# Performance work log

Hardware: AMD Instinct MI355X
Metric: run time of the kernel (lower is better)

The kernel has to match this reference:

```python
import jax, jax.numpy as jnp
import numpy as np

D_MODEL = 768
N_HEADS = 12
D_HEAD = D_MODEL // N_HEADS


def setup_inputs() -> dict:
    key = jax.random.key(0)
    k1, k2, k3 = jax.random.split(key, 3)
    B, N = 32, 1024
    x = jax.random.normal(k1, (B, N, D_MODEL), dtype=jnp.float32)
    w_qkv = jax.random.normal(k2, (D_MODEL, 3 * D_MODEL), dtype=jnp.float32) * (D_MODEL ** -0.5)
    b_qkv = jnp.zeros((3 * D_MODEL,), dtype=jnp.float32)
    w_proj = jax.random.normal(k3, (D_MODEL, D_MODEL), dtype=jnp.float32) * (D_MODEL ** -0.5)
    b_proj = jnp.zeros((D_MODEL,), dtype=jnp.float32)
    return {"x": x, "w_qkv": w_qkv, "b_qkv": b_qkv, "w_proj": w_proj, "b_proj": b_proj}


def reference(x, w_qkv, b_qkv, w_proj, b_proj):
    B, N, C = x.shape
    H, Dh = N_HEADS, D_HEAD
    # qkv projection: (B,N,3C) -> (3,B,H,N,Dh)
    qkv = (x @ w_qkv + b_qkv).reshape(B, N, 3, H, Dh).transpose(2, 0, 3, 1, 4)
    q, k, v = qkv[0], qkv[1], qkv[2]
    scale = Dh ** -0.5
    attn = jnp.einsum('bhnd,bhmd->bhnm', q, k) * scale  # (B,H,N,N)
    attn = jax.nn.softmax(attn, axis=-1)
    out = jnp.einsum('bhnm,bhmd->bhnd', attn, v)  # (B,H,N,Dh)
    out = out.transpose(0, 2, 1, 3).reshape(B, N, C)
    return out @ w_proj + b_proj
```

## Files before the change

kernel.cpp:

```cpp
#include <hip/hip_runtime.h>
#include <hip/hip_bf16.h>
#include <math.h>

#define BQ   32
#define SEQ  1024
#define DM   768
#define NH   12
#define DH   64
#define CQKV 2304
#define MROWS (BQ * SEQ)
#define NT   12

#define QSCALE 0.1803368801f

typedef __attribute__((ext_vector_type(8))) short  short8;
typedef __attribute__((ext_vector_type(4))) short  short4v;
typedef __attribute__((ext_vector_type(4))) float  floatx4;

using bf16 = __hip_bfloat16;

#define G2L(g, l) __builtin_amdgcn_global_load_lds(                              \
        (const __attribute__((address_space(1))) void*)(g),                      \
        (__attribute__((address_space(3))) void*)(l), 16, 0, 0)

#define WAVE_SYNC() __builtin_amdgcn_wave_barrier()
#define MFMA16(a, b, c) __builtin_amdgcn_mfma_f32_16x16x32_bf16((a), (b), (c), 0, 0, 0)

__global__ void cast_f32_bf16(const float* __restrict__ in, bf16* __restrict__ out,
                              int n4)
{
    int idx = blockIdx.x * blockDim.x + threadIdx.x;
    if (idx < n4) {
        float4 v = ((const float4*)in)[idx];
        bf16 o[4] = { __float2bfloat16(v.x), __float2bfloat16(v.y),
                      __float2bfloat16(v.z), __float2bfloat16(v.w) };
        ((ushort4*)out)[idx] = *(const ushort4*)o;
    }
}

__global__ void transpose_cast(const float* __restrict__ in, bf16* __restrict__ out,
                               int R, int C)
{
    int idx = blockIdx.x * blockDim.x + threadIdx.x;
    if (idx < R * C) {
        int r = idx / C, c = idx % C;
        out[(size_t)c * R + r] = __float2bfloat16(in[idx]);
    }
}

__device__ __forceinline__ void mainloop256(
    const bf16* __restrict__ X, const bf16* __restrict__ WT,
    int m0, int n0, int w, int lane, int lr, int lq,
    bf16 (*Asm)[256][64], bf16 (*Bsm)[128][64], floatx4 acc[4][4])
{
    const int wm = (w >> 1) * 64, wn = (w & 1) * 64;
    const int sr = lane >> 3;
    const int ss = ((lane & 7) ^ sr) * 8;
    const bf16* gA = X  + (size_t)(m0 + w * 8 + sr) * DM + ss;
    const bf16* gB = WT + (size_t)(n0 + w * 8 + sr) * DM + ss;

    auto stage = [&](int T) {
        const int bI = T % 3;
        #pragma unroll
        for (int r = 0; r < 4; ++r)
            G2L(gA + (size_t)(r * 64) * DM + T * 64, &Asm[bI][r * 64 + w * 8][0]);
        #pragma unroll
        for (int r = 0; r < 2; ++r)
            G2L(gB + (size_t)(r * 64) * DM + T * 64, &Bsm[bI][r * 64 + w * 8][0]);
    };

    stage(0); stage(1);

    #pragma unroll
    for (int T = 0; T < NT; ++T) {
        if (T + 2 < NT) stage(T + 2);
        if      (T < NT - 2)  asm volatile("s_waitcnt vmcnt(12)" ::: "memory");
        else if (T == NT - 2) asm volatile("s_waitcnt vmcnt(6)"  ::: "memory");
        else                  asm volatile("s_waitcnt vmcnt(0)"  ::: "memory");
        __builtin_amdgcn_s_barrier();
        asm volatile("" ::: "memory");

        const int bI = T % 3;
        short8 af[4][2], bfr[4][2];
        #pragma unroll
        for (int m = 0; m < 4; ++m)
            #pragma unroll
            for (int ks = 0; ks < 2; ++ks)
                af[m][ks] = *(const short8*)(
                    &Asm[bI][wm + m * 16 + lr][((ks * 4 + lq) ^ (lr & 7)) * 8]);
        #pragma unroll
        for (int n = 0; n < 4; ++n)
            #pragma unroll
            for (int ks = 0; ks < 2; ++ks)
                bfr[n][ks] = *(const short8*)(
                    &Bsm[bI][wn + n * 16 + lr][((ks * 4 + lq) ^ (lr & 7)) * 8]);

        __builtin_amdgcn_s_setprio(1);
        #pragma unroll
        for (int ks = 0; ks < 2; ++ks)
            #pragma unroll
            for (int m = 0; m < 4; ++m)
                #pragma unroll
                for (int n = 0; n < 4; ++n)
                    acc[m][n] = MFMA16(af[m][ks], bfr[n][ks], acc[m][n]);
        __builtin_amdgcn_s_setprio(0);

        asm volatile("" ::: "memory");
        __builtin_amdgcn_s_barrier();
        asm volatile("" ::: "memory");
    }
}

__global__ __launch_bounds__(512, 2) void gemm_qkv(
    const bf16* __restrict__ X, const bf16* __restrict__ WT,
    const float* __restrict__ bias,
    bf16* __restrict__ Qo, bf16* __restrict__ Ko, bf16* __restrict__ Vt)
{
    extern __shared__ __align__(16) char smem[];
    auto Asm = (bf16(*)[256][64])smem;
    auto Bsm = (bf16(*)[128][64])(smem + 3 * 256 * 64 * 2);
    auto Es  = (bf16(*)[32][72])smem;

    const int t = threadIdx.x, w = t >> 6, lane = t & 63;
    const int lr = lane & 15, lq = lane >> 4;
    const int id = blockIdx.x;
    const int xcd = id & 7, o = id >> 3;
    const int m0 = (xcd * 16 + o / 18) * 256;
    const int n0 = (o % 18) * 128;

    floatx4 acc[4][4] = {};
    mainloop256(X, WT, m0, n0, w, lane, lr, lq, Asm, Bsm, acc);

    const int wm = (w >> 1) * 64, wn = (w & 1) * 64;
    const int cb = n0 + wn;
    const int which = cb / DM;
    const int hb    = (cb % DM) / DH;
    const int nbw   = m0 + wm;
    const int bb    = nbw >> 10, nloc = nbw & (SEQ - 1);
    const size_t head = (size_t)bb * NH + hb;
    const float qmul = (which == 0) ? QSCALE : 1.0f;

    if (which != 2) {
        bf16* Out = (which ? Ko : Qo) + (head * SEQ + nloc) * DH;
        #pragma unroll
        for (int c2 = 0; c2 < 2; ++c2) {
            #pragma unroll
            for (int ah = 0; ah < 2; ++ah) {
                const int at = c2 * 2 + ah;
                #pragma unroll
                for (int bt = 0; bt < 4; ++bt) {
                    const float bv = bias[cb + bt * 16 + lr];
                    #pragma unroll
                    for (int rr = 0; rr < 4; ++rr)
                        Es[w][ah * 16 + lq * 4 + rr][bt * 16 + lr] =
                            __float2bfloat16((acc[at][bt][rr] + bv) * qmul);
                }
            }
            WAVE_SYNC();
            #pragma unroll
            for (int i = 0; i < 4; ++i) {
                const int r = i * 8 + (lane >> 3), s = lane & 7;
                short8 vv = *(const short8*)(&Es[w][r][s * 8]);
                *(short8*)(Out + (size_t)(c2 * 32 + r) * DH + s * 8) = vv;
            }
            WAVE_SYNC();
        }
    } else {
        bf16* Out = Vt + head * DH * SEQ + nloc;
        #pragma unroll
        for (int c2 = 0; c2 < 2; ++c2) {
            #pragma unroll
            for (int bh = 0; bh < 2; ++bh) {
                const int bt = c2 * 2 + bh;
                const float bv = bias[cb + bt * 16 + lr];
                #pragma unroll
                for (int at = 0; at < 4; ++at)
                    #pragma unroll
                    for (int rr = 0; rr < 4; ++rr)
                        Es[w][bh * 16 + lr][at * 16 + lq * 4 + rr] =
                            __float2bfloat16(acc[at][bt][rr] + bv);
            }
            WAVE_SYNC();
            #pragma unroll
            for (int i = 0; i < 4; ++i) {
                const int r = i * 8 + (lane >> 3), s = lane & 7;
                short8 vv = *(const short8*)(&Es[w][r][s * 8]);
                *(short8*)(Out + (size_t)(c2 * 32 + r) * SEQ + s * 8) = vv;
            }
            WAVE_SYNC();
        }
    }
}

__global__ __launch_bounds__(512, 2) void gemm_proj(
    const bf16* __restrict__ A, const bf16* __restrict__ WT,
    const float* __restrict__ bias, float* __restrict__ out)
{
    extern __shared__ __align__(16) char smem[];
    auto Asm = (bf16(*)[256][64])smem;
    auto Bsm = (bf16(*)[128][64])(smem + 3 * 256 * 64 * 2);

    const int t = threadIdx.x, w = t >> 6, lane = t & 63;
    const int lr = lane & 15, lq = lane >> 4;
    const int id = blockIdx.x;
    const int xcd = id & 7, o = id >> 3;
    const int m0 = (xcd * 16 + o / 6) * 256;
    const int n0 = (o % 6) * 128;

    floatx4 acc[4][4] = {};
    mainloop256(A, WT, m0, n0, w, lane, lr, lq, Asm, Bsm, acc);

    const int wm = (w >> 1) * 64, wn = (w & 1) * 64;
    #pragma unroll
    for (int bt = 0; bt < 4; ++bt) {
        const float bv = bias[n0 + wn + bt * 16 + lr];
        #pragma unroll
        for (int at = 0; at < 4; ++at) {
            const int rg = m0 + wm + at * 16 + lq * 4;
            #pragma unroll
            for (int rr = 0; rr < 4; ++rr)
                out[(size_t)(rg + rr) * DM + n0 + wn + bt * 16 + lr] =
                    acc[at][bt][rr] + bv;
        }
    }
}

__global__ __launch_bounds__(256) void flash_attn(
    const bf16* __restrict__ Q, const bf16* __restrict__ K,
    const bf16* __restrict__ Vt, bf16* __restrict__ O)
{
    __shared__ __align__(16) bf16 Ks[2][2][64][32];
    __shared__ __align__(16) bf16 Vs[2][2][64][32];
    __shared__ __align__(16) bf16 Plds[4][32][72];
    const int w = threadIdx.x >> 6, lane = threadIdx.x & 63;
    const int lr = lane & 15, lq = lane >> 4;

    const int fid = blockIdx.x;
    const int g   = (fid & 7) + ((fid >> 6) << 3);
    const int x   = (fid >> 3) & 7;
    const int h   = g % NH, b = g / NH;
    const int qb  = x * 128 + w * 32;

    const bf16* Qh = Q  + (size_t)(b * NH + h) * SEQ * DH;
    const bf16* Kh = K  + (size_t)(b * NH + h) * SEQ * DH;
    const bf16* Vh = Vt + (size_t)(b * NH + h) * DH * SEQ;

    short8 bq[2][2];
    #pragma unroll
    for (int qs = 0; qs < 2; ++qs) {
        bq[qs][0] = *(const short8*)(Qh + (size_t)(qb + qs * 16 + lr) * DH + lq * 8);
        bq[qs][1] = *(const short8*)(Qh + (size_t)(qb + qs * 16 + lr) * DH + 32 + lq * 8);
    }

    floatx4 acc[2][4] = {};
    floatx4 lsum[2] = {};

    const int srow = lane >> 2;
    const int ssw  = ((lane & 3) ^ ((lane >> 3) & 3)) * 8;
    const int rsw  = (lr >> 1) & 3;

    const bf16* gsrc[4];
    bf16*       ldst[4];
    #pragma unroll
    for (int i = 0; i < 4; ++i) {
        const int idx = w * 4 + i;
        if (idx < 8) {
            const int hh = idx >> 2, gg = idx & 3;
            gsrc[i] = Kh + (size_t)(gg * 16 + srow) * DH + hh * 32 + ssw;
            ldst[i] = &Ks[0][hh][gg * 16][0];
        } else {
            const int vv = idx - 8, hh = vv >> 2, gg = vv & 3;
            gsrc[i] = Vh + (size_t)(gg * 16 + srow) * SEQ + hh * 32 + ssw;
            ldst[i] = &Vs[0][hh][gg * 16][0];
        }
    }
    const int gstep = (w < 2) ? 64 * DH : 64;

    auto stage = [&](int bi) {
        #pragma unroll
        for (int i = 0; i < 4; ++i) {
            G2L(gsrc[i], ldst[i] + bi * 4096);
            gsrc[i] += gstep;
        }
    };

    stage(0);
    __syncthreads();

    int cur = 0;
    for (int j0 = 0; j0 < SEQ; j0 += 64) {
        if (j0 + 64 < SEQ) stage(cur ^ 1);

        short8 ak[4][2];
        #pragma unroll
        for (int jt = 0; jt < 4; ++jt) {
            ak[jt][0] = *(const short8*)(&Ks[cur][0][jt * 16 + lr][(lq ^ rsw) * 8]);
            ak[jt][1] = *(const short8*)(&Ks[cur][1][jt * 16 + lr][(lq ^ rsw) * 8]);
        }
        #pragma unroll
        for (int qs = 0; qs < 2; ++qs) {
            #pragma unroll
            for (int jt = 0; jt < 4; ++jt) {
                floatx4 c = {};
                c = MFMA16(ak[jt][0], bq[qs][0], c);
                c = MFMA16(ak[jt][1], bq[qs][1], c);
                bf16 pk[4];
                #pragma unroll
                for (int r = 0; r < 4; ++r) {
                    float p = __builtin_amdgcn_exp2f(c[r]);
                    lsum[qs][r] += p;
                    pk[r] = __float2bfloat16(p);
                }
                *(short4v*)(&Plds[w][qs * 16 + lr][jt * 16 + lq * 4]) =
                    *(const short4v*)pk;
            }
        }
        WAVE_SYNC();

        short8 bv[4][2];
        #pragma unroll
        for (int dt = 0; dt < 4; ++dt) {
            bv[dt][0] = *(const short8*)(&Vs[cur][0][dt * 16 + lr][(lq ^ rsw) * 8]);
            bv[dt][1] = *(const short8*)(&Vs[cur][1][dt * 16 + lr][(lq ^ rsw) * 8]);
        }
        __builtin_amdgcn_s_setprio(1);
        #pragma unroll
        for (int qs = 0; qs < 2; ++qs) {
            short8 ap0 = *(const short8*)(&Plds[w][qs * 16 + lr][lq * 8]);
            short8 ap1 = *(const short8*)(&Plds[w][qs * 16 + lr][32 + lq * 8]);
            #pragma unroll
            for (int dt = 0; dt < 4; ++dt) {
                acc[qs][dt] = MFMA16(ap0, bv[dt][0], acc[qs][dt]);
                acc[qs][dt] = MFMA16(ap1, bv[dt][1], acc[qs][dt]);
            }
        }
        __builtin_amdgcn_s_setprio(0);

        __syncthreads();
        cur ^= 1;
    }

    float li[2];
    #pragma unroll
    for (int qs = 0; qs < 2; ++qs) {
        li[qs] = (lsum[qs][0] + lsum[qs][1]) + (lsum[qs][2] + lsum[qs][3]);
        li[qs] += __shfl_xor(li[qs], 16);
        li[qs] += __shfl_xor(li[qs], 32);
    }
    #pragma unroll
    for (int qs = 0; qs < 2; ++qs) {
        float inv[4];
        #pragma unroll
        for (int r = 0; r < 4; ++r)
            inv[r] = 1.f / __shfl(li[qs], lq * 4 + r);
        #pragma unroll
        for (int dt = 0; dt < 4; ++dt)
            #pragma unroll
            for (int r = 0; r < 4; ++r) {
                const int qi = qb + qs * 16 + lq * 4 + r;
                O[((size_t)b * SEQ + qi) * DM + h * DH + dt * 16 + lr] =
                    __float2bfloat16(acc[qs][dt][r] * inv[r]);
            }
    }
}

extern "C" void kernel_launch(void* const* d_in, const int* in_sizes, int n_in,
                              void* d_out, int out_size, void* d_ws, size_t ws_size,
                              hipStream_t stream)
{
    const float* x      = (const float*)d_in[0];
    const float* w_qkv  = (const float*)d_in[1];
    const float* b_qkv  = (const float*)d_in[2];
    const float* w_proj = (const float*)d_in[3];
    const float* b_proj = (const float*)d_in[4];
    float* out = (float*)d_out;

    bf16* ws = (bf16*)d_ws;
    size_t off = 0;
    bf16* wqkvT  = ws + off; off += (size_t)CQKV * DM;
    bf16* wprojT = ws + off; off += (size_t)DM * DM;
    bf16* Xb  = ws + off; off += (size_t)MROWS * DM;
    bf16* Qb  = ws + off; off += (size_t)BQ * NH * SEQ * DH;
    bf16* Kb  = ws + off; off += (size_t)BQ * NH * SEQ * DH;
    bf16* Vtb = ws + off; off += (size_t)BQ * NH * DH * SEQ;
    bf16* Ob  = ws + off; off += (size_t)MROWS * DM;

    static bool attr_done = false;
    if (!attr_done) {
        (void)hipFuncSetAttribute((const void*)gemm_qkv,
                hipFuncAttributeMaxDynamicSharedMemorySize, 147456);
        (void)hipFuncSetAttribute((const void*)gemm_proj,
                hipFuncAttributeMaxDynamicSharedMemorySize, 147456);
        attr_done = true;
    }

    cast_f32_bf16<<<(MROWS * DM / 4 + 255) / 256, 256, 0, stream>>>(x, Xb, MROWS * DM / 4);
    transpose_cast<<<(DM * CQKV + 255) / 256, 256, 0, stream>>>(w_qkv, wqkvT, DM, CQKV);
    transpose_cast<<<(DM * DM + 255) / 256, 256, 0, stream>>>(w_proj, wprojT, DM, DM);
    gemm_qkv<<<dim3(2304), 512, 147456, stream>>>(Xb, wqkvT, b_qkv, Qb, Kb, Vtb);
    flash_attn<<<dim3(BQ * NH * (SEQ / 128)), 256, 0, stream>>>(Qb, Kb, Vtb, Ob);
    gemm_proj<<<dim3(768), 512, 147456, stream>>>(Ob, wprojT, b_proj, out);
}
```

Measured before the change: 505.6 us.

## Enlarge GEMM tiles to 256x256 with double-buffered LDS staging

Both projection GEMMs move from 256x128 block tiles with triple-buffered LDS to 256x256 tiles with double buffering. Each wave now owns a 128x64 sub-tile with an 8x4 accumulator array, and the QKV and projection epilogues, including the transposed V store, are rewritten for the new mapping. The goal is more MFMA work per loaded byte and fewer blocks. In exchange, prefetch depth drops, register pressure rises, and the projection grid becomes 384 blocks, which may leave a partial-wave tail.

```diff
diff --git a/kernel.cpp b/kernel.cpp
--- a/kernel.cpp
+++ b/kernel.cpp
@@ -51,55 +51,57 @@
 __device__ __forceinline__ void mainloop256(
     const bf16* __restrict__ X, const bf16* __restrict__ WT,
     int m0, int n0, int w, int lane, int lr, int lq,
-    bf16 (*Asm)[256][64], bf16 (*Bsm)[128][64], floatx4 acc[4][4])
-{
-    const int wm = (w >> 1) * 64, wn = (w & 1) * 64;
+    bf16 (*Asm)[256][64], bf16 (*Bsm)[256][64], floatx4 acc[8][4])
+{
+    const int wm = (w >> 2) * 128, wn = (w & 3) * 64;
+    const int lr7 = lr & 7;
     const int sr = lane >> 3;
     const int ss = ((lane & 7) ^ sr) * 8;
     const bf16* gA = X  + (size_t)(m0 + w * 8 + sr) * DM + ss;
     const bf16* gB = WT + (size_t)(n0 + w * 8 + sr) * DM + ss;
 
     auto stage = [&](int T) {
-        const int bI = T % 3;
+        const int bI = T & 1;
         #pragma unroll
         for (int r = 0; r < 4; ++r)
             G2L(gA + (size_t)(r * 64) * DM + T * 64, &Asm[bI][r * 64 + w * 8][0]);
         #pragma unroll
-        for (int r = 0; r < 2; ++r)
+        for (int r = 0; r < 4; ++r)
             G2L(gB + (size_t)(r * 64) * DM + T * 64, &Bsm[bI][r * 64 + w * 8][0]);
     };
 
-    stage(0); stage(1);
+    stage(0);
 
     #pragma unroll
     for (int T = 0; T < NT; ++T) {
-        if (T + 2 < NT) stage(T + 2);
-        if      (T < NT - 2)  asm volatile("s_waitcnt vmcnt(12)" ::: "memory");
-        else if (T == NT - 2) asm volatile("s_waitcnt vmcnt(6)"  ::: "memory");
-        else                  asm volatile("s_waitcnt vmcnt(0)"  ::: "memory");
+        if (T + 1 < NT) {
+            stage(T + 1);
+            asm volatile("s_waitcnt vmcnt(8)" ::: "memory");
+        } else {
+            asm volatile("s_waitcnt vmcnt(0)" ::: "memory");
+        }
         __builtin_amdgcn_s_barrier();
         asm volatile("" ::: "memory");
 
-        const int bI = T % 3;
-        short8 af[4][2], bfr[4][2];
-        #pragma unroll
-        for (int m = 0; m < 4; ++m)
-            #pragma unroll
-            for (int ks = 0; ks < 2; ++ks)
+        const int bI = T & 1;
+        short8 af[8][2], bfr[4][2];
+        #pragma unroll
+        for (int ks = 0; ks < 2; ++ks) {
+            #pragma unroll
+            for (int m = 0; m < 8; ++m)
                 af[m][ks] = *(const short8*)(
-                    &Asm[bI][wm + m * 16 + lr][((ks * 4 + lq) ^ (lr & 7)) * 8]);
-        #pragma unroll
-        for (int n = 0; n < 4; ++n)
-            #pragma unroll
-            for (int ks = 0; ks < 2; ++ks)
+                    &Asm[bI][wm + m * 16 + lr][((ks * 4 + lq) ^ lr7) * 8]);
+            #pragma unroll
+            for (int n = 0; n < 4; ++n)
                 bfr[n][ks] = *(const short8*)(
-                    &Bsm[bI][wn + n * 16 + lr][((ks * 4 + lq) ^ (lr & 7)) * 8]);
+                    &Bsm[bI][wn + n * 16 + lr][((ks * 4 + lq) ^ lr7) * 8]);
+        }
 
         __builtin_amdgcn_s_setprio(1);
         #pragma unroll
         for (int ks = 0; ks < 2; ++ks)
             #pragma unroll
-            for (int m = 0; m < 4; ++m)
+            for (int m = 0; m < 8; ++m)
                 #pragma unroll
                 for (int n = 0; n < 4; ++n)
                     acc[m][n] = MFMA16(af[m][ks], bfr[n][ks], acc[m][n]);
@@ -118,20 +120,20 @@
 {
     extern __shared__ __align__(16) char smem[];
     auto Asm = (bf16(*)[256][64])smem;
-    auto Bsm = (bf16(*)[128][64])(smem + 3 * 256 * 64 * 2);
-    auto Es  = (bf16(*)[32][72])smem;
+    auto Bsm = (bf16(*)[256][64])(smem + 2 * 256 * 64 * 2);
+    auto Es  = (bf16(*)[64][72])smem;
 
     const int t = threadIdx.x, w = t >> 6, lane = t & 63;
     const int lr = lane & 15, lq = lane >> 4;
     const int id = blockIdx.x;
     const int xcd = id & 7, o = id >> 3;
-    const int m0 = (xcd * 16 + o / 18) * 256;
-    const int n0 = (o % 18) * 128;
-
-    floatx4 acc[4][4] = {};
+    const int m0 = (xcd * 16 + o / 9) * 256;
+    const int n0 = (o % 9) * 256;
+
+    floatx4 acc[8][4] = {};
     mainloop256(X, WT, m0, n0, w, lane, lr, lq, Asm, Bsm, acc);
 
-    const int wm = (w >> 1) * 64, wn = (w & 1) * 64;
+    const int wm = (w >> 2) * 128, wn = (w & 3) * 64;
     const int cb = n0 + wn;
     const int which = cb / DM;
     const int hb    = (cb % DM) / DH;
@@ -143,17 +145,17 @@
     if (which != 2) {
         bf16* Out = (which ? Ko : Qo) + (head * SEQ + nloc) * DH;
         #pragma unroll
-        for (int c2 = 0; c2 < 2; ++c2) {
+        for (int c2 = 0; c2 < 4; ++c2) {
             #pragma unroll
             for (int ah = 0; ah < 2; ++ah) {
-                const int at = c2 * 2 + ah;
+                const int m = c2 * 2 + ah;
                 #pragma unroll
-                for (int bt = 0; bt < 4; ++bt) {
-                    const float bv = bias[cb + bt * 16 + lr];
+                for (int n = 0; n < 4; ++n) {
+                    const float bv = bias[cb + n * 16 + lr];
                     #pragma unroll
                     for (int rr = 0; rr < 4; ++rr)
-                        Es[w][ah * 16 + lq * 4 + rr][bt * 16 + lr] =
-                            __float2bfloat16((acc[at][bt][rr] + bv) * qmul);
+                        Es[w][ah * 16 + lq * 4 + rr][n * 16 + lr] =
+                            __float2bfloat16((acc[m][n][rr] + bv) * qmul);
                 }
             }
             WAVE_SYNC();
@@ -166,26 +168,27 @@
             WAVE_SYNC();
         }
     } else {
-        bf16* Out = Vt + head * DH * SEQ + nloc;
-        #pragma unroll
-        for (int c2 = 0; c2 < 2; ++c2) {
-            #pragma unroll
-            for (int bh = 0; bh < 2; ++bh) {
-                const int bt = c2 * 2 + bh;
-                const float bv = bias[cb + bt * 16 + lr];
+        bf16* Out = Vt + head * (size_t)(DH * SEQ) + nloc;
+        #pragma unroll
+        for (int mc = 0; mc < 4; ++mc) {
+            #pragma unroll
+            for (int ah = 0; ah < 2; ++ah) {
+                const int m = mc * 2 + ah;
                 #pragma unroll
-                for (int at = 0; at < 4; ++at)
+                for (int n = 0; n < 4; ++n) {
+                    const float bv = bias[cb + n * 16 + lr];
                     #pragma unroll
                     for (int rr = 0; rr < 4; ++rr)
-                        Es[w][bh * 16 + lr][at * 16 + lq * 4 + rr] =
-                            __float2bfloat16(acc[at][bt][rr] + bv);
+                        Es[w][n * 16 + lr][ah * 16 + lq * 4 + rr] =
+                            __float2bfloat16(acc[m][n][rr] + bv);
+                }
             }
             WAVE_SYNC();
             #pragma unroll
             for (int i = 0; i < 4; ++i) {
-                const int r = i * 8 + (lane >> 3), s = lane & 7;
+                const int r = i * 16 + (lane >> 2), s = lane & 3;
                 short8 vv = *(const short8*)(&Es[w][r][s * 8]);
-                *(short8*)(Out + (size_t)(c2 * 32 + r) * SEQ + s * 8) = vv;
+                *(short8*)(Out + (size_t)r * SEQ + mc * 32 + s * 8) = vv;
             }
             WAVE_SYNC();
         }
@@ -198,29 +201,29 @@
 {
     extern __shared__ __align__(16) char smem[];
     auto Asm = (bf16(*)[256][64])smem;
-    auto Bsm = (bf16(*)[128][64])(smem + 3 * 256 * 64 * 2);
+    auto Bsm = (bf16(*)[256][64])(smem + 2 * 256 * 64 * 2);
 
     const int t = threadIdx.x, w = t >> 6, lane = t & 63;
     const int lr = lane & 15, lq = lane >> 4;
     const int id = blockIdx.x;
     const int xcd = id & 7, o = id >> 3;
-    const int m0 = (xcd * 16 + o / 6) * 256;
-    const int n0 = (o % 6) * 128;
-
-    floatx4 acc[4][4] = {};
+    const int m0 = (xcd * 16 + o / 3) * 256;
+    const int n0 = (o % 3) * 256;
+
+    floatx4 acc[8][4] = {};
     mainloop256(A, WT, m0, n0, w, lane, lr, lq, Asm, Bsm, acc);
 
-    const int wm = (w >> 1) * 64, wn = (w & 1) * 64;
-    #pragma unroll
-    for (int bt = 0; bt < 4; ++bt) {
-        const float bv = bias[n0 + wn + bt * 16 + lr];
-        #pragma unroll
-        for (int at = 0; at < 4; ++at) {
-            const int rg = m0 + wm + at * 16 + lq * 4;
+    const int wm = (w >> 2) * 128, wn = (w & 3) * 64;
+    #pragma unroll
+    for (int n = 0; n < 4; ++n) {
+        const float bv = bias[n0 + wn + n * 16 + lr];
+        #pragma unroll
+        for (int m = 0; m < 8; ++m) {
+            const int rg = m0 + wm + m * 16 + lq * 4;
             #pragma unroll
             for (int rr = 0; rr < 4; ++rr)
-                out[(size_t)(rg + rr) * DM + n0 + wn + bt * 16 + lr] =
-                    acc[at][bt][rr] + bv;
+                out[(size_t)(rg + rr) * DM + n0 + wn + n * 16 + lr] =
+                    acc[m][n][rr] + bv;
         }
     }
 }
@@ -388,16 +391,16 @@
     static bool attr_done = false;
     if (!attr_done) {
         (void)hipFuncSetAttribute((const void*)gemm_qkv,
-                hipFuncAttributeMaxDynamicSharedMemorySize, 147456);
+                hipFuncAttributeMaxDynamicSharedMemorySize, 131072);
         (void)hipFuncSetAttribute((const void*)gemm_proj,
-                hipFuncAttributeMaxDynamicSharedMemorySize, 147456);
+                hipFuncAttributeMaxDynamicSharedMemorySize, 131072);
         attr_done = true;
     }
 
     cast_f32_bf16<<<(MROWS * DM / 4 + 255) / 256, 256, 0, stream>>>(x, Xb, MROWS * DM / 4);
     transpose_cast<<<(DM * CQKV + 255) / 256, 256, 0, stream>>>(w_qkv, wqkvT, DM, CQKV);
     transpose_cast<<<(DM * DM + 255) / 256, 256, 0, stream>>>(w_proj, wprojT, DM, DM);
-    gemm_qkv<<<dim3(2304), 512, 147456, stream>>>(Xb, wqkvT, b_qkv, Qb, Kb, Vtb);
+    gemm_qkv<<<dim3(1152), 512, 131072, stream>>>(Xb, wqkvT, b_qkv, Qb, Kb, Vtb);
     flash_attn<<<dim3(BQ * NH * (SEQ / 128)), 256, 0, stream>>>(Qb, Kb, Vtb, Ob);
-    gemm_proj<<<dim3(768), 512, 147456, stream>>>(Ob, wprojT, b_proj, out);
-}
+    gemm_proj<<<dim3(384), 512, 131072, stream>>>(Ob, wprojT, b_proj, out);
+}
```

New measurement: 500.8 us. About the same (-0.9%).
